# Optimization experiments

Hardware: AMD Instinct MI355X
Metric: run time of the kernel (lower is better)

The kernel has to match this reference:

```python
import jax, jax.numpy as jnp
import numpy as np

E2M1_GRID = jnp.array([0.0, 0.5, 1.0, 1.5, 2.0, 3.0, 4.0, 6.0], dtype=jnp.float32)
E2M1_MIDS = (E2M1_GRID[1:] + E2M1_GRID[:-1]) / 2.0
FP4_MAX = 6.0
FP8_E4M3_MAX = 448.0


def nvfp4_quant_dequant(w):
    # Emulates tetrajetv2.quant_fp4_dequant_trans_fused: two-level scaling
    # (fp32 outer scale per 128 inputs, fp8-e4m3 inner scale per 16 inputs),
    # values rounded to the signed E2M1 grid, then dequantized.
    O, I = w.shape
    w16 = w.reshape(O, I // 128, 8, 16)
    amax128 = jnp.max(jnp.abs(w16), axis=(-2, -1))          # [O, I/128]
    outer = amax128 / (FP4_MAX * FP8_E4M3_MAX)
    outer = jnp.where(outer > 0, outer, 1.0)
    amax16 = jnp.max(jnp.abs(w16), axis=-1)                  # [O, I/128, 8]
    inner = amax16 / FP4_MAX / outer[..., None]
    inner = inner.astype(jnp.float8_e4m3fn).astype(jnp.float32)  # fp8 round
    scale = outer[..., None] * inner                          # [O, I/128, 8]
    safe = jnp.where(scale > 0, scale, 1.0)[..., None]
    code = w16 / safe
    a = jnp.abs(code)
    idx = jnp.searchsorted(E2M1_MIDS, a)                      # nearest grid pt
    q = E2M1_GRID[idx] * jnp.sign(code)
    return (q * scale[..., None]).reshape(O, I)


def setup_inputs() -> dict:
    key = jax.random.key(0)
    k0, k1, k2 = jax.random.split(key, 3)
    B, S, H = 2, 2048, 2048
    hidden_states = jax.random.normal(k0, (B, S, H), dtype=jnp.float32)
    # raw weights ~ N(0, 0.023) as in FP4Linear init, then fake-quantized
    w_qkv = jax.random.normal(k1, (3 * H, H), dtype=jnp.float32) * 0.023
    w_o = jax.random.normal(k2, (H, H), dtype=jnp.float32) * 0.023
    w_qkv = nvfp4_quant_dequant(w_qkv)
    w_o = nvfp4_quant_dequant(w_o)
    return {"hidden_states": hidden_states, "w_qkv": w_qkv, "w_o": w_o}


def reference(hidden_states, w_qkv, w_o):
    B, S, H = hidden_states.shape
    num_heads = 16
    head_dim = H // num_heads
    qkv = jnp.einsum('bsh,oh->bso', hidden_states, w_qkv)      # [B,S,3H]
    qkv = qkv.reshape(B, S, 3, num_heads, head_dim)
    qkv = jnp.transpose(qkv, (2, 0, 3, 1, 4))                  # [3,B,nh,S,hd]
    q, k, v = qkv[0], qkv[1], qkv[2]
    scale = 1.0 / jnp.sqrt(jnp.float32(head_dim))
    scores = jnp.einsum('bhqd,bhkd->bhqk', q, k) * scale
    causal = jnp.tril(jnp.ones((S, S), dtype=bool))
    scores = jnp.where(causal, scores, jnp.finfo(scores.dtype).min)
    probs = jax.nn.softmax(scores, axis=-1)
    attn = jnp.einsum('bhqk,bhkd->bhqd', probs, v)             # [B,nh,S,hd]
    attn = jnp.transpose(attn, (0, 2, 1, 3)).reshape(B, S, H)
    return jnp.einsum('bsh,oh->bso', attn, w_o)
```

## Files before the change

kernel.cpp:

```cpp
#include <hip/hip_runtime.h>
#include <hip/hip_bf16.h>
#include <stdint.h>

typedef __bf16 bf16x8 __attribute__((ext_vector_type(8)));
typedef float f32x4 __attribute__((ext_vector_type(4)));

#define AS1 __attribute__((address_space(1)))
#define AS3 __attribute__((address_space(3)))

#define PBAR() do { __builtin_amdgcn_sched_barrier(0); asm volatile("s_barrier" ::: "memory"); __builtin_amdgcn_sched_barrier(0); } while (0)
#define LGK0() do { asm volatile("s_waitcnt lgkmcnt(0)" ::: "memory"); __builtin_amdgcn_sched_barrier(0); } while (0)
#define VMCNT(n) do { asm volatile("s_waitcnt vmcnt(" #n ")" ::: "memory"); __builtin_amdgcn_sched_barrier(0); } while (0)

__device__ __forceinline__ unsigned short f2bf(float x) {
    union { float f; uint32_t u; } v; v.f = x;
    uint32_t r = v.u + 0x7fffu + ((v.u >> 16) & 1u);
    return (unsigned short)(r >> 16);
}

__global__ void k_f2bf(const float* __restrict__ in, unsigned short* __restrict__ out, int n4) {
    int i = blockIdx.x * blockDim.x + threadIdx.x;
    if (i >= n4) return;
    float4 v = reinterpret_cast<const float4*>(in)[i];
    ushort4 o;
    o.x = f2bf(v.x); o.y = f2bf(v.y); o.z = f2bf(v.z); o.w = f2bf(v.w);
    reinterpret_cast<ushort4*>(out)[i] = o;
}

__global__ __launch_bounds__(512, 2) void k_gemm256x256(
    const unsigned short* __restrict__ A,
    const unsigned short* __restrict__ B,
    unsigned short* __restrict__ C, int M, int N, int K, int ngrid)
{
    __shared__ __align__(16) unsigned short Al[2][8192];
    __shared__ __align__(16) unsigned short Bl[2][8192];
    const int tid = threadIdx.x, lane = tid & 63, wv = tid >> 6;
    const int wr = wv >> 2, wc = wv & 3;
    const int fl = lane & 15, fg = lane >> 4;
    const int cpx = ngrid >> 3;
    const int sw = ((int)blockIdx.x & 7) * cpx + ((int)blockIdx.x >> 3);
    const int bm = sw & 15, bn = sw >> 4;
    const int nK = K >> 5;

    const unsigned short* Ag = A + (size_t)bm * 256 * K;
    const unsigned short* Bg = B + (size_t)bn * 256 * K;

    auto stage = [&](int buf, int t) {
#pragma unroll
        for (int u = 0; u < 2; ++u) {
            int ch = u * 512 + tid;
            int r = ch >> 2, cs = (ch & 3) ^ ((r >> 1) & 3);
            __builtin_amdgcn_global_load_lds(
                (const AS1 void*)(Ag + (size_t)r * K + t * 32 + cs * 8),
                (AS3 void*)((char*)&Al[buf][0] + ch * 16), 16, 0, 0);
        }
#pragma unroll
        for (int u = 0; u < 2; ++u) {
            int ch = u * 512 + tid;
            int r = ch >> 2, cs = (ch & 3) ^ ((r >> 1) & 3);
            __builtin_amdgcn_global_load_lds(
                (const AS1 void*)(Bg + (size_t)r * K + t * 32 + cs * 8),
                (AS3 void*)((char*)&Bl[buf][0] + ch * 16), 16, 0, 0);
        }
    };
    auto ldfrag = [&](const unsigned short* base, int r) -> bf16x8 {
        return *reinterpret_cast<const bf16x8*>(
            (const char*)base + r * 64 + ((fg ^ ((r >> 1) & 3)) << 4));
    };

    f32x4 acc[8][4];
#pragma unroll
    for (int i = 0; i < 8; ++i)
#pragma unroll
        for (int j = 0; j < 4; ++j) acc[i][j] = (f32x4){0.f, 0.f, 0.f, 0.f};

    stage(0, 0);
    VMCNT(0);
    PBAR();

    for (int t = 0; t < nK; ++t) {
        const int c = t & 1;
        if (t + 1 < nK) stage(c ^ 1, t + 1);
        __builtin_amdgcn_sched_barrier(0);
        bf16x8 af[8], bv[4];
#pragma unroll
        for (int i = 0; i < 8; ++i) af[i] = ldfrag(Al[c], wr * 128 + i * 16 + fl);
#pragma unroll
        for (int j = 0; j < 4; ++j) bv[j] = ldfrag(Bl[c], wc * 64 + j * 16 + fl);
        LGK0();
        __builtin_amdgcn_s_setprio(1);
#pragma unroll
        for (int i = 0; i < 8; ++i)
#pragma unroll
            for (int j = 0; j < 4; ++j)
                acc[i][j] = __builtin_amdgcn_mfma_f32_16x16x32_bf16(af[i], bv[j], acc[i][j], 0, 0, 0);
        __builtin_amdgcn_s_setprio(0);
        if (t + 1 < nK) { VMCNT(0); }
        PBAR();
    }

#pragma unroll
    for (int i = 0; i < 8; ++i)
#pragma unroll
        for (int j = 0; j < 4; ++j)
#pragma unroll
            for (int r = 0; r < 4; ++r) {
                int row = bm * 256 + wr * 128 + i * 16 + fg * 4 + r;
                int col = bn * 256 + wc * 64 + j * 16 + fl;
                C[(size_t)row * N + col] = f2bf(acc[i][j][r]);
            }
}

template <typename TOUT>
__global__ __launch_bounds__(512, 2) void k_gemm128x256(
    const unsigned short* __restrict__ A,
    const unsigned short* __restrict__ B,
    TOUT* __restrict__ C, int M, int N, int K, int ngrid)
{
    __shared__ __align__(16) unsigned short Albuf[3][4096];
    __shared__ __align__(16) unsigned short Blbuf[3][8192];
    const int tid = threadIdx.x, lane = tid & 63, wv = tid >> 6;
    const int wr = wv >> 2, wc = wv & 3;
    const int fl = lane & 15, fg = lane >> 4;
    const int cpx = ngrid >> 3;
    const int sw = ((int)blockIdx.x & 7) * cpx + ((int)blockIdx.x >> 3);
    const int bm = sw & 31, bn = sw >> 5;
    const int nK = K >> 5;

    const unsigned short* Ag = A + (size_t)bm * 128 * K;
    const unsigned short* Bg = B + (size_t)bn * 256 * K;

    auto stageA = [&](int buf, int t) {
        const int r = tid >> 2;
        const int cs = (tid & 3) ^ ((r >> 1) & 3);
        const unsigned short* src = Ag + (size_t)r * K + t * 32 + cs * 8;
        __builtin_amdgcn_global_load_lds((const AS1 void*)src,
            (AS3 void*)((char*)&Albuf[buf][0] + wv * 1024), 16, 0, 0);
    };
    auto stageB = [&](int buf, int half, int t) {
        const int r = tid >> 2;
        const int cs = (tid & 3) ^ ((r >> 1) & 3);
        const unsigned short* src = Bg + (size_t)(half * 128 + r) * K + t * 32 + cs * 8;
        __builtin_amdgcn_global_load_lds((const AS1 void*)src,
            (AS3 void*)((char*)&Blbuf[buf][0] + half * 8192 + wv * 1024), 16, 0, 0);
    };
    auto ldfrag = [&](const unsigned short* base, int r) -> bf16x8 {
        return *reinterpret_cast<const bf16x8*>(
            (const char*)base + r * 64 + ((fg ^ ((r >> 1) & 3)) << 4));
    };

    f32x4 acc[4][4];
#pragma unroll
    for (int i = 0; i < 4; ++i)
#pragma unroll
        for (int j = 0; j < 4; ++j) acc[i][j] = (f32x4){0.f, 0.f, 0.f, 0.f};

    stageA(0, 0); stageB(0, 0, 0); stageB(0, 1, 0);
    stageA(1, 1); stageB(1, 0, 1); stageB(1, 1, 1);
    asm volatile("s_waitcnt vmcnt(3)" ::: "memory");
    PBAR();

    int c = 0;
    for (int t = 0; t < nK; ++t) {
        const unsigned short* Ac = Albuf[c];
        const unsigned short* Bc = Blbuf[c];
        bf16x8 af[4], bv[4];
#pragma unroll
        for (int i = 0; i < 4; ++i) af[i] = ldfrag(Ac, wr * 64 + i * 16 + fl);
#pragma unroll
        for (int j = 0; j < 4; ++j) bv[j] = ldfrag(Bc, wc * 64 + j * 16 + fl);
        if (t + 2 < nK) {
            int nb = c + 2; if (nb >= 3) nb -= 3;
            stageA(nb, t + 2); stageB(nb, 0, t + 2); stageB(nb, 1, t + 2);
        }
        PBAR();
        LGK0();
        __builtin_amdgcn_s_setprio(1);
#pragma unroll
        for (int i = 0; i < 4; ++i)
#pragma unroll
            for (int j = 0; j < 4; ++j)
                acc[i][j] = __builtin_amdgcn_mfma_f32_16x16x32_bf16(af[i], bv[j], acc[i][j], 0, 0, 0);
        __builtin_amdgcn_s_setprio(0);
        if (t + 2 < nK)      { asm volatile("s_waitcnt vmcnt(3)" ::: "memory"); }
        else if (t + 1 < nK) { asm volatile("s_waitcnt vmcnt(0)" ::: "memory"); }
        PBAR();
        ++c; if (c == 3) c = 0;
    }

#pragma unroll
    for (int i = 0; i < 4; ++i)
#pragma unroll
        for (int j = 0; j < 4; ++j)
#pragma unroll
            for (int r = 0; r < 4; ++r) {
                int row = bm * 128 + wr * 64 + i * 16 + fg * 4 + r;
                int col = bn * 256 + wc * 64 + j * 16 + fl;
                float v = acc[i][j][r];
                if constexpr (sizeof(TOUT) == 2)
                    ((unsigned short*)C)[(size_t)row * N + col] = f2bf(v);
                else
                    C[(size_t)row * N + col] = v;
            }
}

__global__ void k_transpose_v(const unsigned short* __restrict__ qkv, unsigned short* __restrict__ vT) {
    __shared__ unsigned short t[32][33];
    const int bh = blockIdx.z;
    const int b = bh >> 4, h = bh & 15;
    const int s0 = blockIdx.x * 32, d0 = blockIdx.y * 32;
    const int tx = threadIdx.x, ty = threadIdx.y;
#pragma unroll
    for (int i = 0; i < 4; ++i) {
        int s = s0 + ty + i * 8;
        t[ty + i * 8][tx] = qkv[(size_t)(b * 2048 + s) * 6144 + 4096 + h * 128 + d0 + tx];
    }
    __syncthreads();
#pragma unroll
    for (int i = 0; i < 4; ++i) {
        int d = d0 + ty + i * 8;
        vT[((size_t)bh * 128 + d) * 2048 + s0 + tx] = t[tx][ty + i * 8];
    }
}

__global__ __launch_bounds__(256, 2) void k_attn(
    const unsigned short* __restrict__ qkv, const unsigned short* __restrict__ vT,
    unsigned short* __restrict__ out)
{
    __shared__ unsigned short Klds[2][8192];
    __shared__ unsigned short Vlds[8192];
    __shared__ __align__(16) unsigned short Plds[4][2048];

    const int tid = threadIdx.x, lane = tid & 63, wv = tid >> 6;
    const int fl = lane & 15, fg = lane >> 4;
    const int bh = blockIdx.y;
    const int qb = (bh >= 16) ? blockIdx.x : 15 - blockIdx.x;
    const int b = bh >> 4, h = bh & 15;
    const int q0w = qb * 128 + wv * 32;
    const size_t base = (size_t)b * 2048 * 6144 + (size_t)h * 128;
    const unsigned short* Qbase = qkv + base;
    const unsigned short* Kbase = qkv + base + 2048;
    const unsigned short* Vbase = vT + (size_t)bh * 128 * 2048;
    unsigned short* pw = Plds[wv];

    bf16x8 qf[2][4];
#pragma unroll
    for (int m = 0; m < 2; ++m)
#pragma unroll
        for (int kk = 0; kk < 4; ++kk)
            qf[m][kk] = *reinterpret_cast<const bf16x8*>(
                Qbase + (size_t)(q0w + m * 16 + fl) * 6144 + kk * 32 + fg * 8);
    asm volatile("s_waitcnt vmcnt(0)" ::: "memory");
    __builtin_amdgcn_sched_barrier(0);

    auto stageK = [&](int buf, int kv0) {
#pragma unroll
        for (int rnd = 0; rnd < 4; ++rnd) {
            int ch = rnd * 256 + tid;
            int row = ch >> 4;
            int cbl = ((ch & 15) << 4) ^ ((row & 7) << 4);
            const unsigned short* src = Kbase + (size_t)(kv0 + row) * 6144 + (cbl >> 1);
            __builtin_amdgcn_global_load_lds((const AS1 void*)src,
                (AS3 void*)((char*)&Klds[buf][0] + (rnd * 256 + wv * 64) * 16), 16, 0, 0);
        }
    };
    auto stageV = [&](int kv0) {
#pragma unroll
        for (int rnd = 0; rnd < 4; ++rnd) {
            int ch = rnd * 256 + tid;
            int row = ch >> 3;
            int cbl = ((ch & 7) << 4) ^ ((row & 7) << 4);
            const unsigned short* src = Vbase + (size_t)row * 2048 + kv0 + (cbl >> 1);
            __builtin_amdgcn_global_load_lds((const AS1 void*)src,
                (AS3 void*)((char*)&Vlds[0] + (rnd * 256 + wv * 64) * 16), 16, 0, 0);
        }
    };

    f32x4 acc[2][8];
#pragma unroll
    for (int m = 0; m < 2; ++m)
#pragma unroll
        for (int nb = 0; nb < 8; ++nb) acc[m][nb] = (f32x4){0.f, 0.f, 0.f, 0.f};
    float l_r[2] = {0.f, 0.f};
    const float sc = 0.08838834764831845f;
    const int nIter = 2 * qb + 2;

    stageK(0, 0);

    for (int it = 0; it < nIter; ++it) {
        const int kv0 = it * 64;
        const bool act = (kv0 <= q0w + 31);
        const bool haveK = (it + 1 < nIter);
        stageV(kv0);
        if (haveK) stageK((it + 1) & 1, kv0 + 64);
        __builtin_amdgcn_sched_barrier(0);
        if (haveK) { VMCNT(8); } else { VMCNT(4); }
        PBAR();
        if (act) {
            const bool full = (kv0 + 63 <= q0w);
            const unsigned short* Kb = Klds[it & 1];
            f32x4 s[2][4];
#pragma unroll
            for (int m = 0; m < 2; ++m)
#pragma unroll
                for (int n = 0; n < 4; ++n) s[m][n] = (f32x4){0.f, 0.f, 0.f, 0.f};
            __builtin_amdgcn_s_setprio(1);
#pragma unroll
            for (int kk = 0; kk < 4; ++kk)
#pragma unroll
                for (int n = 0; n < 4; ++n) {
                    const int row = n * 16 + fl;
                    bf16x8 kf = *reinterpret_cast<const bf16x8*>(
                        (const char*)Kb + row * 256 + ((kk * 64 + fg * 16) ^ ((row & 7) << 4)));
                    s[0][n] = __builtin_amdgcn_mfma_f32_16x16x32_bf16(kf, qf[0][kk], s[0][n], 0, 0, 0);
                    s[1][n] = __builtin_amdgcn_mfma_f32_16x16x32_bf16(kf, qf[1][kk], s[1][n], 0, 0, 0);
                }
            __builtin_amdgcn_s_setprio(0);
#pragma unroll
            for (int m = 0; m < 2; ++m) {
                const int qi = q0w + m * 16 + fl;
                const int prow = m * 16 + fl;
                const int rb = prow * 128, swz = (prow & 7) << 4;
#pragma unroll
                for (int n = 0; n < 4; ++n) {
                    const int kbase = kv0 + n * 16 + fg * 4;
                    float v0 = s[m][n][0] * sc, v1 = s[m][n][1] * sc,
                          v2 = s[m][n][2] * sc, v3 = s[m][n][3] * sc;
                    if (!full) {
                        if (kbase     > qi) v0 = -3e38f;
                        if (kbase + 1 > qi) v1 = -3e38f;
                        if (kbase + 2 > qi) v2 = -3e38f;
                        if (kbase + 3 > qi) v3 = -3e38f;
                    }
                    float p0 = __expf(v0 - 10.f), p1 = __expf(v1 - 10.f),
                          p2 = __expf(v2 - 10.f), p3 = __expf(v3 - 10.f);
                    l_r[m] += p0 + p1 + p2 + p3;
                    uint32_t lo = (uint32_t)f2bf(p0) | ((uint32_t)f2bf(p1) << 16);
                    uint32_t hi = (uint32_t)f2bf(p2) | ((uint32_t)f2bf(p3) << 16);
                    const int byte = rb + ((n * 32 + fg * 8) ^ swz);
                    uint2 pk; pk.x = lo; pk.y = hi;
                    *reinterpret_cast<uint2*>((char*)pw + byte) = pk;
                }
            }
            LGK0();
        }
        if (haveK) { VMCNT(4); } else { VMCNT(0); }
        PBAR();
        if (act) {
            bf16x8 pf[2][2];
#pragma unroll
            for (int m = 0; m < 2; ++m)
#pragma unroll
                for (int k2 = 0; k2 < 2; ++k2) {
                    const int row = m * 16 + fl;
                    pf[m][k2] = *reinterpret_cast<const bf16x8*>(
                        (const char*)pw + row * 128 + ((k2 * 64 + fg * 16) ^ ((row & 7) << 4)));
                }
            __builtin_amdgcn_s_setprio(1);
#pragma unroll
            for (int nb = 0; nb < 8; ++nb)
#pragma unroll
                for (int k2 = 0; k2 < 2; ++k2) {
                    const int d = nb * 16 + fl;
                    bf16x8 vf = *reinterpret_cast<const bf16x8*>(
                        (const char*)Vlds + d * 128 + ((k2 * 64 + fg * 16) ^ ((d & 7) << 4)));
                    acc[0][nb] = __builtin_amdgcn_mfma_f32_16x16x32_bf16(pf[0][k2], vf, acc[0][nb], 0, 0, 0);
                    acc[1][nb] = __builtin_amdgcn_mfma_f32_16x16x32_bf16(pf[1][k2], vf, acc[1][nb], 0, 0, 0);
                }
            __builtin_amdgcn_s_setprio(0);
        }
        PBAR();
    }

#pragma unroll
    for (int m = 0; m < 2; ++m) {
        float l = l_r[m];
        l += __shfl_xor(l, 16);
        l += __shfl_xor(l, 32);
        float inv[4];
#pragma unroll
        for (int r = 0; r < 4; ++r) inv[r] = 1.0f / __shfl(l, fg * 4 + r);
#pragma unroll
        for (int nb = 0; nb < 8; ++nb)
#pragma unroll
            for (int r = 0; r < 4; ++r) {
                int row = q0w + m * 16 + fg * 4 + r;
                int col = h * 128 + nb * 16 + fl;
                out[(size_t)(b * 2048 + row) * 2048 + col] = f2bf(acc[m][nb][r] * inv[r]);
            }
    }
}

extern "C" void kernel_launch(void* const* d_in, const int* in_sizes, int n_in,
                              void* d_out, int out_size, void* d_ws, size_t ws_size,
                              hipStream_t stream) {
    const float* hs   = (const float*)d_in[0];
    const float* wqkv = (const float*)d_in[1];
    const float* wo   = (const float*)d_in[2];
    float* out = (float*)d_out;

    char* p = (char*)d_ws;
    unsigned short* Xb    = (unsigned short*)p; p += (size_t)4096 * 2048 * 2;
    unsigned short* Wqkvb = (unsigned short*)p; p += (size_t)6144 * 2048 * 2;
    unsigned short* Wob   = (unsigned short*)p; p += (size_t)2048 * 2048 * 2;
    unsigned short* QKV   = (unsigned short*)p; p += (size_t)4096 * 6144 * 2;
    unsigned short* VT    = (unsigned short*)p; p += (size_t)32 * 128 * 2048 * 2;
    unsigned short* ATTN  = (unsigned short*)p; p += (size_t)4096 * 2048 * 2;

    k_f2bf<<<8192, 256, 0, stream>>>(hs, Xb, 2097152);
    k_f2bf<<<12288, 256, 0, stream>>>(wqkv, Wqkvb, 3145728);
    k_f2bf<<<4096, 256, 0, stream>>>(wo, Wob, 1048576);
    k_gemm256x256<<<384, 512, 0, stream>>>(Xb, Wqkvb, QKV, 4096, 6144, 2048, 384);
    k_transpose_v<<<dim3(64, 4, 32), dim3(32, 8), 0, stream>>>(QKV, VT);
    k_attn<<<dim3(16, 32), 256, 0, stream>>>(QKV, VT, ATTN);
    k_gemm128x256<float><<<256, 512, 0, stream>>>(ATTN, Wob, out, 4096, 2048, 2048, 256);
}
```

Measured before the change: 301.3 us.

## Fuse bf16 conversions, retile QKV and output-projection GEMMs for better occupancy

```diff
diff --git a/kernel.cpp b/kernel.cpp
--- a/kernel.cpp
+++ b/kernel.cpp
@@ -18,97 +18,19 @@
     return (unsigned short)(r >> 16);
 }
 
-__global__ void k_f2bf(const float* __restrict__ in, unsigned short* __restrict__ out, int n4) {
+__global__ void k_f2bf3(const float* __restrict__ a, unsigned short* __restrict__ oa, int na4,
+                        const float* __restrict__ b, unsigned short* __restrict__ ob, int nb4,
+                        const float* __restrict__ c, unsigned short* __restrict__ oc, int nc4) {
     int i = blockIdx.x * blockDim.x + threadIdx.x;
-    if (i >= n4) return;
-    float4 v = reinterpret_cast<const float4*>(in)[i];
+    const float* src; unsigned short* dst; int j;
+    if (i < na4)            { src = a; dst = oa; j = i; }
+    else if (i < na4 + nb4) { src = b; dst = ob; j = i - na4; }
+    else if (i < na4 + nb4 + nc4) { src = c; dst = oc; j = i - na4 - nb4; }
+    else return;
+    float4 v = reinterpret_cast<const float4*>(src)[j];
     ushort4 o;
     o.x = f2bf(v.x); o.y = f2bf(v.y); o.z = f2bf(v.z); o.w = f2bf(v.w);
-    reinterpret_cast<ushort4*>(out)[i] = o;
-}
-
-__global__ __launch_bounds__(512, 2) void k_gemm256x256(
-    const unsigned short* __restrict__ A,
-    const unsigned short* __restrict__ B,
-    unsigned short* __restrict__ C, int M, int N, int K, int ngrid)
-{
-    __shared__ __align__(16) unsigned short Al[2][8192];
-    __shared__ __align__(16) unsigned short Bl[2][8192];
-    const int tid = threadIdx.x, lane = tid & 63, wv = tid >> 6;
-    const int wr = wv >> 2, wc = wv & 3;
-    const int fl = lane & 15, fg = lane >> 4;
-    const int cpx = ngrid >> 3;
-    const int sw = ((int)blockIdx.x & 7) * cpx + ((int)blockIdx.x >> 3);
-    const int bm = sw & 15, bn = sw >> 4;
-    const int nK = K >> 5;
-
-    const unsigned short* Ag = A + (size_t)bm * 256 * K;
-    const unsigned short* Bg = B + (size_t)bn * 256 * K;
-
-    auto stage = [&](int buf, int t) {
-#pragma unroll
-        for (int u = 0; u < 2; ++u) {
-            int ch = u * 512 + tid;
-            int r = ch >> 2, cs = (ch & 3) ^ ((r >> 1) & 3);
-            __builtin_amdgcn_global_load_lds(
-                (const AS1 void*)(Ag + (size_t)r * K + t * 32 + cs * 8),
-                (AS3 void*)((char*)&Al[buf][0] + ch * 16), 16, 0, 0);
-        }
-#pragma unroll
-        for (int u = 0; u < 2; ++u) {
-            int ch = u * 512 + tid;
-            int r = ch >> 2, cs = (ch & 3) ^ ((r >> 1) & 3);
-            __builtin_amdgcn_global_load_lds(
-                (const AS1 void*)(Bg + (size_t)r * K + t * 32 + cs * 8),
-                (AS3 void*)((char*)&Bl[buf][0] + ch * 16), 16, 0, 0);
-        }
-    };
-    auto ldfrag = [&](const unsigned short* base, int r) -> bf16x8 {
-        return *reinterpret_cast<const bf16x8*>(
-            (const char*)base + r * 64 + ((fg ^ ((r >> 1) & 3)) << 4));
-    };
-
-    f32x4 acc[8][4];
-#pragma unroll
-    for (int i = 0; i < 8; ++i)
-#pragma unroll
-        for (int j = 0; j < 4; ++j) acc[i][j] = (f32x4){0.f, 0.f, 0.f, 0.f};
-
-    stage(0, 0);
-    VMCNT(0);
-    PBAR();
-
-    for (int t = 0; t < nK; ++t) {
-        const int c = t & 1;
-        if (t + 1 < nK) stage(c ^ 1, t + 1);
-        __builtin_amdgcn_sched_barrier(0);
-        bf16x8 af[8], bv[4];
-#pragma unroll
-        for (int i = 0; i < 8; ++i) af[i] = ldfrag(Al[c], wr * 128 + i * 16 + fl);
-#pragma unroll
-        for (int j = 0; j < 4; ++j) bv[j] = ldfrag(Bl[c], wc * 64 + j * 16 + fl);
-        LGK0();
-        __builtin_amdgcn_s_setprio(1);
-#pragma unroll
-        for (int i = 0; i < 8; ++i)
-#pragma unroll
-            for (int j = 0; j < 4; ++j)
-                acc[i][j] = __builtin_amdgcn_mfma_f32_16x16x32_bf16(af[i], bv[j], acc[i][j], 0, 0, 0);
-        __builtin_amdgcn_s_setprio(0);
-        if (t + 1 < nK) { VMCNT(0); }
-        PBAR();
-    }
-
-#pragma unroll
-    for (int i = 0; i < 8; ++i)
-#pragma unroll
-        for (int j = 0; j < 4; ++j)
-#pragma unroll
-            for (int r = 0; r < 4; ++r) {
-                int row = bm * 256 + wr * 128 + i * 16 + fg * 4 + r;
-                int col = bn * 256 + wc * 64 + j * 16 + fl;
-                C[(size_t)row * N + col] = f2bf(acc[i][j][r]);
-            }
+    reinterpret_cast<ushort4*>(dst)[j] = o;
 }
 
 template <typename TOUT>
@@ -201,6 +123,98 @@
                     ((unsigned short*)C)[(size_t)row * N + col] = f2bf(v);
                 else
                     C[(size_t)row * N + col] = v;
+            }
+}
+
+__global__ __launch_bounds__(256, 3) void k_gemm128x128(
+    const unsigned short* __restrict__ A,
+    const unsigned short* __restrict__ B,
+    float* __restrict__ C, int M, int N, int K, int ngrid)
+{
+    __shared__ __align__(16) unsigned short Al[3][4096];
+    __shared__ __align__(16) unsigned short Bl[3][4096];
+    const int tid = threadIdx.x, lane = tid & 63, wv = tid >> 6;
+    const int wr = wv >> 1, wc = wv & 1;
+    const int fl = lane & 15, fg = lane >> 4;
+    const int cpx = ngrid >> 3;
+    const int sw = ((int)blockIdx.x & 7) * cpx + ((int)blockIdx.x >> 3);
+    const int bm = sw & 31, bn = sw >> 5;
+    const int nK = K >> 5;
+
+    const unsigned short* Ag = A + (size_t)bm * 128 * K;
+    const unsigned short* Bg = B + (size_t)bn * 128 * K;
+
+    auto stage = [&](int buf, int t) {
+#pragma unroll
+        for (int u = 0; u < 2; ++u) {
+            int ch = u * 256 + tid;
+            int r = ch >> 2, cs = (ch & 3) ^ ((r >> 1) & 3);
+            __builtin_amdgcn_global_load_lds(
+                (const AS1 void*)(Ag + (size_t)r * K + t * 32 + cs * 8),
+                (AS3 void*)((char*)&Al[buf][0] + (u * 256 + wv * 64) * 16), 16, 0, 0);
+        }
+#pragma unroll
+        for (int u = 0; u < 2; ++u) {
+            int ch = u * 256 + tid;
+            int r = ch >> 2, cs = (ch & 3) ^ ((r >> 1) & 3);
+            __builtin_amdgcn_global_load_lds(
+                (const AS1 void*)(Bg + (size_t)r * K + t * 32 + cs * 8),
+                (AS3 void*)((char*)&Bl[buf][0] + (u * 256 + wv * 64) * 16), 16, 0, 0);
+        }
+    };
+    auto ldfrag = [&](const unsigned short* base, int r) -> bf16x8 {
+        return *reinterpret_cast<const bf16x8*>(
+            (const char*)base + r * 64 + ((fg ^ ((r >> 1) & 3)) << 4));
+    };
+
+    f32x4 acc[4][4];
+#pragma unroll
+    for (int i = 0; i < 4; ++i)
+#pragma unroll
+        for (int j = 0; j < 4; ++j) acc[i][j] = (f32x4){0.f, 0.f, 0.f, 0.f};
+
+    stage(0, 0);
+    stage(1, 1);
+    asm volatile("s_waitcnt vmcnt(4)" ::: "memory");
+    PBAR();
+
+    int c = 0;
+    for (int t = 0; t < nK; ++t) {
+        const unsigned short* Ac = Al[c];
+        const unsigned short* Bc = Bl[c];
+        bf16x8 af[4], bv[4];
+#pragma unroll
+        for (int i = 0; i < 4; ++i) af[i] = ldfrag(Ac, wr * 64 + i * 16 + fl);
+#pragma unroll
+        for (int j = 0; j < 4; ++j) bv[j] = ldfrag(Bc, wc * 64 + j * 16 + fl);
+        if (t + 2 < nK) {
+            int nb = c + 2; if (nb >= 3) nb -= 3;
+            stage(nb, t + 2);
+        }
+        PBAR();
+        LGK0();
+        __builtin_amdgcn_s_setprio(1);
+#pragma unroll
+        for (int i = 0; i < 4; ++i)
+#pragma unroll
+            for (int j = 0; j < 4; ++j)
+                acc[i][j] = __builtin_amdgcn_mfma_f32_16x16x32_bf16(af[i], bv[j], acc[i][j], 0, 0, 0);
+        __builtin_amdgcn_s_setprio(0);
+        if (t + 2 < nK)      { asm volatile("s_waitcnt vmcnt(4)" ::: "memory"); }
+        else if (t + 1 < nK) { asm volatile("s_waitcnt vmcnt(0)" ::: "memory"); }
+        PBAR();
+        ++c; if (c == 3) c = 0;
+    }
+
+#pragma unroll
+    for (int i = 0; i < 4; ++i)
+#pragma unroll
+        for (int j = 0; j < 4; ++j)
+#pragma unroll
+            for (int r = 0; r < 4; ++r) {
+                int row = bm * 128 + wr * 64 + i * 16 + fg * 4 + r;
+                int col = bn * 128 + wc * 64 + j * 16 + fl;
+                C[(size_t)row * N + col] = acc[i][j][r];
             }
 }
 
@@ -407,11 +421,9 @@
     unsigned short* VT    = (unsigned short*)p; p += (size_t)32 * 128 * 2048 * 2;
     unsigned short* ATTN  = (unsigned short*)p; p += (size_t)4096 * 2048 * 2;
 
-    k_f2bf<<<8192, 256, 0, stream>>>(hs, Xb, 2097152);
-    k_f2bf<<<12288, 256, 0, stream>>>(wqkv, Wqkvb, 3145728);
-    k_f2bf<<<4096, 256, 0, stream>>>(wo, Wob, 1048576);
-    k_gemm256x256<<<384, 512, 0, stream>>>(Xb, Wqkvb, QKV, 4096, 6144, 2048, 384);
+    k_f2bf3<<<24576, 256, 0, stream>>>(hs, Xb, 2097152, wqkv, Wqkvb, 3145728, wo, Wob, 1048576);
+    k_gemm128x256<unsigned short><<<768, 512, 0, stream>>>(Xb, Wqkvb, QKV, 4096, 6144, 2048, 768);
     k_transpose_v<<<dim3(64, 4, 32), dim3(32, 8), 0, stream>>>(QKV, VT);
     k_attn<<<dim3(16, 32), 256, 0, stream>>>(QKV, VT, ATTN);
-    k_gemm128x256<float><<<256, 512, 0, stream>>>(ATTN, Wob, out, 4096, 2048, 2048, 256);
-}
+    k_gemm128x128<<<512, 256, 0, stream>>>(ATTN, Wob, out, 4096, 2048, 2048, 512);
+}
```

Result: faster. 255.4 us (-15.2%).
